# Performance work log

Hardware: AMD Instinct MI355X
Metric: run time of the kernel (lower is better)

Reference implementation:

```python
import jax, jax.numpy as jnp
import numpy as np

NBITS = 8
REDUCE = 64
OUT = 512


def setup_inputs() -> dict:
    key = jax.random.key(0)
    ks = jax.random.split(key, 6)
    T, B, C = 512, 16, 512
    ne = 2 ** NBITS
    x = jax.random.normal(ks[0], (T, B, C), dtype=jnp.float32)
    key_in = jax.random.normal(ks[1], (T, B, C), dtype=jnp.float32)  # unused by forward (overwritten)
    # xavier-ish init scales
    map_w = jax.random.normal(ks[2], (NBITS, C), dtype=jnp.float32) * np.sqrt(2.0 / (C + NBITS))
    map_b = jnp.zeros((NBITS,), dtype=jnp.float32)
    pw_w1 = jax.random.normal(ks[3], (REDUCE, C), dtype=jnp.float32) * np.sqrt(2.0 / (C + REDUCE))
    pw_w21 = jax.random.normal(ks[4], (ne, OUT * REDUCE), dtype=jnp.float32) * np.sqrt(2.0 / (ne + OUT * REDUCE))
    pw_w22 = jax.random.normal(ks[5], (ne, OUT * REDUCE), dtype=jnp.float32) * np.sqrt(2.0 / (ne + OUT * REDUCE))
    pw_B = jnp.zeros((1, 1, OUT), dtype=jnp.float32)
    return {"x": x, "key": key_in, "map_w": map_w, "map_b": map_b,
            "pw_w1": pw_w1, "pw_w21": pw_w21, "pw_w22": pw_w22, "pw_B": pw_B}


def reference(x, key, map_w, map_b, pw_w1, pw_w21, pw_w22, pw_B):
    # x: (T,B,C). `key` arg is overwritten by x in the original source.
    T, B, C = x.shape
    nbits = map_w.shape[0]
    out_dim = pw_B.shape[-1]
    reduce_dim = pw_w1.shape[0]

    k = x.reshape(T * B, C) @ map_w.T + map_b          # (T*B, nbits)
    z = jnp.clip(1.2 * jax.nn.sigmoid(k) - 0.1, 0.0, 1.0)  # saturated sigmoid
    code = (z > 0.5).astype(z.dtype)                   # eval: hard binary code

    pows = (2 ** jnp.arange(nbits, dtype=jnp.int32))   # bit_to_int weights
    qz1 = jnp.sum(code.astype(jnp.int32) * pows, axis=-1)          # (T*B,)
    qz2 = jnp.sum((1 - code.astype(jnp.int32)) * pows, axis=-1)    # (T*B,)

    # gather per-token expert rows and synthesize per-token weight matrix
    w2 = (pw_w21[qz1] + pw_w22[qz2]).reshape(T, B, out_dim, reduce_dim)

    # original computes (w2 @ pw_w1) @ x; reassociated as w2 @ (pw_w1 @ x)
    # to avoid materializing the (T,B,out,in) intermediate (same math)
    v = jnp.einsum('ri,tbi->tbr', pw_w1, x)            # (T,B,reduce)
    y = jnp.einsum('tbor,tbr->tbo', w2, v) + pw_B      # (T,B,out)

    loss = jnp.zeros((1,), dtype=x.dtype)
    return (y, loss)
```

## Files before the change

### kernel.cpp

```cpp
#include <hip/hip_runtime.h>

#define NTOK 8192
#define CDIM 512
#define NB   8
#define RD   64
#define OD   512

typedef unsigned char  u8;
typedef unsigned int   u32;
typedef unsigned short u16;

#define WS_Q    0
#define WS_OFF  8192
#define WS_LIST 9728
#define WS_V    26112
#define WS_NEED (WS_V + (size_t)NTOK * RD * 4)

__global__ __launch_bounds__(512) void kA(
    const float* __restrict__ x, const float* __restrict__ map_w,
    const float* __restrict__ map_b, const float* __restrict__ w1,
    u8* __restrict__ q_out, float* __restrict__ v_out,
    float* __restrict__ loss_out)
{
    const int t    = threadIdx.x;
    const int tok0 = blockIdx.x * 16;
    __shared__ float xs[16 * CDIM];
    __shared__ float vs[16 * 68];
    __shared__ u32   qm[8];

    const float4* __restrict__ xsrc = (const float4*)(x + (size_t)tok0 * CDIM);
    #pragma unroll
    for (int u = 0; u < 4; ++u) {
        int g  = u * 512 + t;
        int r  = g >> 7, c4 = g & 127;
        int col = (c4 * 4) ^ ((r & 7) << 3);
        *(float4*)(xs + r * CDIM + col) = xsrc[g];
    }
    __syncthreads();

    const int w    = t >> 6;
    const int lane = t & 63;
    const int tok  = lane & 15;
    const int ch   = lane >> 4;
    const int sw   = (tok & 7) << 3;
    const float* __restrict__ xrow = xs + tok * CDIM;
    const float* __restrict__ wrow = w1 + (size_t)(w * 8) * CDIM;
    const float* __restrict__ mrow = map_w + (size_t)w * CDIM;

    float a[8] = {0.f, 0.f, 0.f, 0.f, 0.f, 0.f, 0.f, 0.f};
    double s = 0.0;

    for (int st = 0; st < 32; ++st) {
        const int c = ch * 128 + st * 4;
        float4 xv = *(const float4*)(xrow + (c ^ sw));
        #pragma unroll
        for (int j = 0; j < 8; ++j) {
            float4 wv = *(const float4*)(wrow + (size_t)j * CDIM + c);
            a[j] += wv.x * xv.x + wv.y * xv.y + wv.z * xv.z + wv.w * xv.w;
        }
        float4 mv = *(const float4*)(mrow + c);
        s += (double)mv.x * (double)xv.x + (double)mv.y * (double)xv.y
           + (double)mv.z * (double)xv.z + (double)mv.w * (double)xv.w;
    }

    #pragma unroll
    for (int j = 0; j < 8; ++j) {
        a[j] += __shfl_xor(a[j], 16);
        a[j] += __shfl_xor(a[j], 32);
    }
    s += __shfl_xor(s, 16);
    s += __shfl_xor(s, 32);
    s += (double)map_b[w];

    unsigned long long mask = __ballot(s > 0.0);
    if (lane == 0) qm[w] = (u32)(mask & 0xFFFFull);

    if (lane < 16) {
        #pragma unroll
        for (int j = 0; j < 8; ++j) vs[tok * 68 + w * 8 + j] = a[j];
    }
    __syncthreads();

    if (t < 16) {
        u32 q = 0;
        #pragma unroll
        for (int b = 0; b < 8; ++b) q |= ((qm[b] >> t) & 1u) << b;
        q_out[tok0 + t] = (u8)q;
    }
    if (t < 256) {
        int tk = t >> 4, j4 = t & 15;
        *(float4*)(v_out + (size_t)(tok0 + tk) * RD + j4 * 4) =
            *(const float4*)(vs + tk * 68 + j4 * 4);
    }
    if (blockIdx.x == 0 && t == 0) loss_out[0] = 0.0f;
}

__global__ __launch_bounds__(1024) void kSort(
    const u8* __restrict__ q_arr, u32* __restrict__ off, u16* __restrict__ list)
{
    __shared__ u32 hist[256], curs[256], scan[256];
    const int t = threadIdx.x;
    if (t < 256) hist[t] = 0u;
    __syncthreads();
    for (int i = t; i < NTOK; i += 1024) atomicAdd(&hist[q_arr[i]], 1u);
    __syncthreads();
    if (t < 256) scan[t] = hist[t];
    __syncthreads();
    for (int d = 1; d < 256; d <<= 1) {
        u32 v = 0u;
        if (t < 256 && t >= d) v = scan[t - d];
        __syncthreads();
        if (t < 256) scan[t] += v;
        __syncthreads();
    }
    if (t < 256) {
        u32 excl = scan[t] - hist[t];
        curs[t] = excl;
        off[t]  = excl;
        if (t == 255) off[256] = scan[255];
    }
    __syncthreads();
    for (int i = t; i < NTOK; i += 1024) {
        u32 pos = atomicAdd(&curs[q_arr[i]], 1u);
        list[pos] = (u16)i;
    }
}

__global__ __launch_bounds__(256) void kB(
    const u16* __restrict__ list, const u32* __restrict__ off,
    const float* __restrict__ v_arr,
    const float* __restrict__ w21, const float* __restrict__ w22,
    const float* __restrict__ pwB, float* __restrict__ y)
{
    const int q  = blockIdx.x >> 1;
    const int oh = blockIdx.x & 1;
    const int t  = threadIdx.x;
    const int o  = oh * 256 + t;
    const u32 lo = off[q], hi = off[q + 1];
    const int n  = (int)(hi - lo);
    if (n == 0) return;

    __shared__ u16 ltok[NTOK];

    const float4* __restrict__ pa = (const float4*)(w21 + ((size_t)q * OD + o) * RD);
    const float4* __restrict__ pb = (const float4*)(w22 + ((size_t)(255 - q) * OD + o) * RD);
    float4 wa[16], wb[16];
    #pragma unroll
    for (int j = 0; j < 16; ++j) wa[j] = pa[j];
    #pragma unroll
    for (int j = 0; j < 16; ++j) wb[j] = pb[j];

    for (int i = t; i < n; i += 256) ltok[i] = list[lo + i];

    float4 w[16];
    #pragma unroll
    for (int j = 0; j < 16; ++j)
        w[j] = make_float4(wa[j].x + wb[j].x, wa[j].y + wb[j].y,
                           wa[j].z + wb[j].z, wa[j].w + wb[j].w);
    const float bias = pwB[o];
    __syncthreads();

    const float4* __restrict__ v4 = (const float4*)v_arr;
    for (int i = 0; i < n; i += 4) {
        const int nb = n - i;
        const int t0 = (int)ltok[i];
        const int t1 = (int)ltok[(nb > 1) ? i + 1 : i];
        const int t2 = (int)ltok[(nb > 2) ? i + 2 : i];
        const int t3 = (int)ltok[(nb > 3) ? i + 3 : i];
        const float4* __restrict__ p0 = v4 + (size_t)t0 * 16;
        const float4* __restrict__ p1 = v4 + (size_t)t1 * 16;
        const float4* __restrict__ p2 = v4 + (size_t)t2 * 16;
        const float4* __restrict__ p3 = v4 + (size_t)t3 * 16;
        float a0 = bias, a1 = bias, a2 = bias, a3 = bias;
        #pragma unroll
        for (int j = 0; j < 16; ++j) {
            float4 ww = w[j];
            float4 v0 = p0[j]; a0 += ww.x*v0.x + ww.y*v0.y + ww.z*v0.z + ww.w*v0.w;
            float4 v1 = p1[j]; a1 += ww.x*v1.x + ww.y*v1.y + ww.z*v1.z + ww.w*v1.w;
            float4 v2 = p2[j]; a2 += ww.x*v2.x + ww.y*v2.y + ww.z*v2.z + ww.w*v2.w;
            float4 v3 = p3[j]; a3 += ww.x*v3.x + ww.y*v3.y + ww.z*v3.z + ww.w*v3.w;
        }
        y[(size_t)t0 * OD + o] = a0;
        if (nb > 1) y[(size_t)t1 * OD + o] = a1;
        if (nb > 2) y[(size_t)t2 * OD + o] = a2;
        if (nb > 3) y[(size_t)t3 * OD + o] = a3;
    }
}

__global__ __launch_bounds__(256) void mono(
    const float* __restrict__ x, const float* __restrict__ map_w,
    const float* __restrict__ map_b, const float* __restrict__ w1,
    const float* __restrict__ w21, const float* __restrict__ w22,
    const float* __restrict__ pwB, float* __restrict__ y)
{
    const int tok = blockIdx.x;
    const int t   = threadIdx.x;
    __shared__ float xsh[CDIM];
    __shared__ float vsh[RD];
    __shared__ int qsh;

    if (t == 0) qsh = 0;
    for (int i = t; i < CDIM; i += 256) xsh[i] = x[(size_t)tok * CDIM + i];
    __syncthreads();

    if (t < NB) {
        double a = 0.0;
        const float* mrow = map_w + (size_t)t * CDIM;
        for (int j = 0; j < CDIM; ++j) a += (double)mrow[j] * (double)xsh[j];
        a += (double)map_b[t];
        if (a > 0.0) atomicOr(&qsh, 1 << t);
    }
    if (t < RD) {
        const float* wrow = w1 + (size_t)t * CDIM;
        float acc = 0.f;
        for (int j = 0; j < CDIM; ++j) acc += wrow[j] * xsh[j];
        vsh[t] = acc;
    }
    __syncthreads();

    const int q = qsh;
    for (int o = t; o < OD; o += 256) {
        const float* pa = w21 + (size_t)q * (OD * RD) + (size_t)o * RD;
        const float* pb = w22 + (size_t)(255 - q) * (OD * RD) + (size_t)o * RD;
        float acc = pwB[o];
        for (int r = 0; r < RD; ++r) acc += (pa[r] + pb[r]) * vsh[r];
        y[(size_t)tok * OD + o] = acc;
    }
    if (tok == 0 && t == 0) y[(size_t)NTOK * OD] = 0.0f;
}

extern "C" void kernel_launch(void* const* d_in, const int* in_sizes, int n_in,
                              void* d_out, int out_size, void* d_ws, size_t ws_size,
                              hipStream_t stream) {
    const float* x     = (const float*)d_in[0];
    const float* map_w = (const float*)d_in[2];
    const float* map_b = (const float*)d_in[3];
    const float* w1    = (const float*)d_in[4];
    const float* w21   = (const float*)d_in[5];
    const float* w22   = (const float*)d_in[6];
    const float* pwB   = (const float*)d_in[7];
    float* out = (float*)d_out;

    if (ws_size >= WS_NEED) {
        char* ws = (char*)d_ws;
        u8*    q_ws   = (u8*)(ws + WS_Q);
        u32*   off    = (u32*)(ws + WS_OFF);
        u16*   list   = (u16*)(ws + WS_LIST);
        float* v_ws   = (float*)(ws + WS_V);

        kA<<<NTOK / 16, 512, 0, stream>>>(x, map_w, map_b, w1, q_ws, v_ws,
                                          out + (size_t)NTOK * OD);
        kSort<<<1, 1024, 0, stream>>>(q_ws, off, list);
        kB<<<512, 256, 0, stream>>>(list, off, v_ws, w21, w22, pwB, out);
    } else {
        mono<<<NTOK, 256, 0, stream>>>(x, map_w, map_b, w1, w21, w22, pwB, out);
    }
}
```

Before: 232.9 us.

## Stage gathered token vectors in LDS and split kB into single-wave blocks

kB now launches 2048 single-wave blocks, each covering 64 output rows for one code, in place of 512 blocks of 256 threads. Each block cooperatively gathers up to 64 token v-vectors into shared memory and then broadcasts them from LDS to all lanes. Before, every thread read the same v rows straight from global or cache memory. This cuts redundant per-lane global loads and spreads work across more CUs, at the cost of extra barriers and reading each block's weights and token list separately.

```diff
diff --git a/kernel.cpp b/kernel.cpp
--- a/kernel.cpp
+++ b/kernel.cpp
@@ -126,64 +126,65 @@
     }
 }
 
-__global__ __launch_bounds__(256) void kB(
+__global__ __launch_bounds__(64) void kB(
     const u16* __restrict__ list, const u32* __restrict__ off,
     const float* __restrict__ v_arr,
     const float* __restrict__ w21, const float* __restrict__ w22,
     const float* __restrict__ pwB, float* __restrict__ y)
 {
-    const int q  = blockIdx.x >> 1;
-    const int oh = blockIdx.x & 1;
-    const int t  = threadIdx.x;
-    const int o  = oh * 256 + t;
-    const u32 lo = off[q], hi = off[q + 1];
-    const int n  = (int)(hi - lo);
+    const int q    = blockIdx.x >> 3;
+    const int og   = blockIdx.x & 7;
+    const int lane = threadIdx.x;
+    const int o    = og * 64 + lane;
+    const u32 lo   = off[q];
+    const int n    = (int)(off[q + 1] - lo);
     if (n == 0) return;
 
-    __shared__ u16 ltok[NTOK];
+    __shared__ float vsl[64 * RD];
+    __shared__ u16   ctok[64];
 
     const float4* __restrict__ pa = (const float4*)(w21 + ((size_t)q * OD + o) * RD);
     const float4* __restrict__ pb = (const float4*)(w22 + ((size_t)(255 - q) * OD + o) * RD);
-    float4 wa[16], wb[16];
-    #pragma unroll
-    for (int j = 0; j < 16; ++j) wa[j] = pa[j];
-    #pragma unroll
-    for (int j = 0; j < 16; ++j) wb[j] = pb[j];
-
-    for (int i = t; i < n; i += 256) ltok[i] = list[lo + i];
-
     float4 w[16];
     #pragma unroll
-    for (int j = 0; j < 16; ++j)
-        w[j] = make_float4(wa[j].x + wb[j].x, wa[j].y + wb[j].y,
-                           wa[j].z + wb[j].z, wa[j].w + wb[j].w);
+    for (int j = 0; j < 16; ++j) {
+        float4 a = pa[j], b = pb[j];
+        w[j] = make_float4(a.x + b.x, a.y + b.y, a.z + b.z, a.w + b.w);
+    }
     const float bias = pwB[o];
-    __syncthreads();
-
     const float4* __restrict__ v4 = (const float4*)v_arr;
-    for (int i = 0; i < n; i += 4) {
-        const int nb = n - i;
-        const int t0 = (int)ltok[i];
-        const int t1 = (int)ltok[(nb > 1) ? i + 1 : i];
-        const int t2 = (int)ltok[(nb > 2) ? i + 2 : i];
-        const int t3 = (int)ltok[(nb > 3) ? i + 3 : i];
-        const float4* __restrict__ p0 = v4 + (size_t)t0 * 16;
-        const float4* __restrict__ p1 = v4 + (size_t)t1 * 16;
-        const float4* __restrict__ p2 = v4 + (size_t)t2 * 16;
-        const float4* __restrict__ p3 = v4 + (size_t)t3 * 16;
-        float a0 = bias, a1 = bias, a2 = bias, a3 = bias;
-        #pragma unroll
-        for (int j = 0; j < 16; ++j) {
-            float4 ww = w[j];
-            float4 v0 = p0[j]; a0 += ww.x*v0.x + ww.y*v0.y + ww.z*v0.z + ww.w*v0.w;
-            float4 v1 = p1[j]; a1 += ww.x*v1.x + ww.y*v1.y + ww.z*v1.z + ww.w*v1.w;
-            float4 v2 = p2[j]; a2 += ww.x*v2.x + ww.y*v2.y + ww.z*v2.z + ww.w*v2.w;
-            float4 v3 = p3[j]; a3 += ww.x*v3.x + ww.y*v3.y + ww.z*v3.z + ww.w*v3.w;
+
+    for (int base = 0; base < n; base += 64) {
+        const int nc = min(64, n - base);
+        ctok[lane] = list[lo + base + min(lane, nc - 1)];
+        __syncthreads();
+        const int tot = nc * 16;
+        for (int i0 = 0; i0 < tot; i0 += 64) {
+            const int i = i0 + lane;
+            if (i < tot) {
+                const int tok = (int)ctok[i >> 4];
+                *(float4*)(vsl + i * 4) = v4[(size_t)tok * 16 + (i & 15)];
+            }
         }
-        y[(size_t)t0 * OD + o] = a0;
-        if (nb > 1) y[(size_t)t1 * OD + o] = a1;
-        if (nb > 2) y[(size_t)t2 * OD + o] = a2;
-        if (nb > 3) y[(size_t)t3 * OD + o] = a3;
+        __syncthreads();
+        for (int c = 0; c < nc; ++c) {
+            const float* vp = vsl + c * RD;
+            float a0 = 0.f, a1 = 0.f, a2 = 0.f, a3 = 0.f;
+            #pragma unroll
+            for (int j = 0; j < 16; j += 4) {
+                float4 v0 = *(const float4*)(vp + (j + 0) * 4);
+                float4 v1 = *(const float4*)(vp + (j + 1) * 4);
+                float4 v2 = *(const float4*)(vp + (j + 2) * 4);
+                float4 v3 = *(const float4*)(vp + (j + 3) * 4);
+                a0 += w[j+0].x*v0.x + w[j+0].y*v0.y + w[j+0].z*v0.z + w[j+0].w*v0.w;
+                a1 += w[j+1].x*v1.x + w[j+1].y*v1.y + w[j+1].z*v1.z + w[j+1].w*v1.w;
+                a2 += w[j+2].x*v2.x + w[j+2].y*v2.y + w[j+2].z*v2.z + w[j+2].w*v2.w;
+                a3 += w[j+3].x*v3.x + w[j+3].y*v3.y + w[j+3].z*v3.z + w[j+3].w*v3.w;
+            }
+            const int tok = (int)ctok[c];
+            y[(size_t)tok * OD + o] = bias + (a0 + a1) + (a2 + a3);
+        }
+        __syncthreads();
     }
 }
 
@@ -251,7 +252,7 @@
         kA<<<NTOK / 16, 512, 0, stream>>>(x, map_w, map_b, w1, q_ws, v_ws,
                                           out + (size_t)NTOK * OD);
         kSort<<<1, 1024, 0, stream>>>(q_ws, off, list);
-        kB<<<512, 256, 0, stream>>>(list, off, v_ws, w21, w22, pwB, out);
+        kB<<<2048, 64, 0, stream>>>(list, off, v_ws, w21, w22, pwB, out);
     } else {
         mono<<<NTOK, 256, 0, stream>>>(x, map_w, map_b, w1, w21, w22, pwB, out);
     }
```

Result: faster. 205.5 us (-11.7%).
